# Optimization experiments

Measured on AMD Instinct MI355X. Metric: run time of the kernel, lower is better.

Reference implementation:

```python
import jax, jax.numpy as jnp
import numpy as np

TAU = 2.0          # LIF membrane time constant
VTH = 1.0          # spike threshold
ALPHA = 2.0        # ATan surrogate default alpha
EPS = 1e-5         # LayerNorm eps


@jax.custom_vjp
def atan_spike(x):
    # Heaviside forward, ATan surrogate gradient backward (spikingjelly surrogate.ATan)
    return (x >= 0.0).astype(x.dtype)

def _spike_fwd(x):
    return atan_spike(x), x

def _spike_bwd(x, g):
    sg = (ALPHA / 2.0) / (1.0 + (jnp.pi / 2.0 * ALPHA * x) ** 2)
    return (g * sg,)

atan_spike.defvjp(_spike_fwd, _spike_bwd)


def lif_scan(xs):
    # xs: [T, B, C]; multi-step LIF with decay_input=True, v_reset=0.0 (hard reset),
    # detach_reset=True (reset path is stop_gradient'ed).
    def step(v, x):
        h = v + (x - v) / TAU                      # charge
        s = atan_spike(h - VTH)                    # fire
        v_new = h * (1.0 - jax.lax.stop_gradient(s))  # hard reset to 0, detached
        return v_new, s
    _, spikes = jax.lax.scan(step, jnp.zeros_like(xs[0]), xs)
    return spikes


def setup_inputs() -> dict:
    key = jax.random.key(0)
    ks = jax.random.split(key, 5)
    B, T, D, H = 32, 2048, 128, 256
    x = jax.random.normal(ks[0], (B, T, D), dtype=jnp.float32)
    W1 = jax.random.normal(ks[1], (H, D), dtype=jnp.float32) * (1.0 / np.sqrt(D))
    b1 = jax.random.normal(ks[2], (H,), dtype=jnp.float32) * 0.02
    W2 = jax.random.normal(ks[3], (D, H), dtype=jnp.float32) * (1.0 / np.sqrt(H))
    b2 = jax.random.normal(ks[4], (D,), dtype=jnp.float32) * 0.02
    ln_w = jnp.ones((D,), dtype=jnp.float32)
    ln_b = jnp.zeros((D,), dtype=jnp.float32)
    return {"x": x, "W1": W1, "b1": b1, "W2": W2, "b2": b2, "ln_w": ln_w, "ln_b": ln_b}


def reference(x, W1, b1, W2, b2, ln_w, ln_b):
    # x: [B, T, D] -> time-major [T, B, D]
    h = jnp.swapaxes(x, 0, 1)
    h = h @ W1.T + b1            # [T, B, H]
    h = lif_scan(h)              # spikes in {0,1}
    h = h @ W2.T + b2            # [T, B, D]
    h = lif_scan(h)
    h = jnp.swapaxes(h, 0, 1)    # back to [B, T, D]
    y = x + h                    # residual
    mu = jnp.mean(y, axis=-1, keepdims=True)
    var = jnp.mean((y - mu) ** 2, axis=-1, keepdims=True)
    return (y - mu) * jax.lax.rsqrt(var + EPS) * ln_w + ln_b
```

## Files before the change

### kernel.cpp

```cpp
#include <hip/hip_runtime.h>


typedef _Float16 half8 __attribute__((ext_vector_type(8)));
typedef float f32x4 __attribute__((ext_vector_type(4)));

#define MFMA_F16(a, b, c) __builtin_amdgcn_mfma_f32_16x16x32_f16(a, b, c, 0, 0, 0)

__device__ __forceinline__ unsigned short h2u(_Float16 h) {
    union { _Float16 h; unsigned short u; } x; x.h = h; return x.u;
}

__device__ __forceinline__ void split8(float4 f0, float4 f1, half8& a, half8& b) {
    float fs[8] = {f0.x, f0.y, f0.z, f0.w, f1.x, f1.y, f1.z, f1.w};
    half8 ha, hb;
#pragma unroll
    for (int q = 0; q < 8; ++q) {
        ha[q] = (_Float16)fs[q];
        hb[q] = (_Float16)(fs[q] - (float)ha[q]);
    }
    a = ha; b = hb;
}

__global__ __launch_bounds__(512, 1) void mega_kernel(
    const float* __restrict__ X,
    const float* __restrict__ W1, const float* __restrict__ W2,
    const float* __restrict__ b1, const float* __restrict__ b2,
    const float* __restrict__ lnw, const float* __restrict__ lnb,
    float* __restrict__ out)
{
    __shared__ __align__(16) float h1buf[16 * 260];
    __shared__ __align__(16) float h2buf[16 * 132];
    __shared__ __align__(16) float s2buf[16 * 132];
    __shared__ __align__(16) unsigned short spkbuf[16 * 264];
    __shared__ __align__(16) unsigned short xb[2][16 * 136];

    const int tid = threadIdx.x;
    const int lane = tid & 63;
    const int w = tid >> 6;
    const bool isS = (tid < 256);
    const int sg = w;
    const int gg = w - 4;
    const int fr = lane & 15;
    const int fo8 = (lane >> 4) * 8;
    const int qr = (lane >> 4) * 4;
    const int b = blockIdx.y;
    const int t0 = blockIdx.x * 256;
    const int s0 = (blockIdx.x == 0) ? 8 : 0;

    const float* __restrict__ xbase = X + (size_t)b * 2048 * 128;
    float* __restrict__ obase = out + (size_t)b * 2048 * 128;

    half8 wf[32];
    float bias0[4];
    if (isS) {
#pragma unroll
        for (int j = 0; j < 2; ++j) {
            const size_t d = (size_t)(32 * sg + 16 * j + fr) * 256;
#pragma unroll
            for (int ks = 0; ks < 8; ++ks) {
                float4 f0 = *(const float4*)&W2[d + ks * 32 + fo8];
                float4 f1 = *(const float4*)&W2[d + ks * 32 + fo8 + 4];
                split8(f0, f1, wf[(j * 8 + ks) * 2], wf[(j * 8 + ks) * 2 + 1]);
            }
            bias0[j] = b2[32 * sg + 16 * j + fr];
        }
    } else {
#pragma unroll
        for (int j = 0; j < 4; ++j) {
            const size_t n = (size_t)(64 * gg + 16 * j + fr) * 128;
#pragma unroll
            for (int k0 = 0; k0 < 4; ++k0) {
                float4 f0 = *(const float4*)&W1[n + k0 * 32 + fo8];
                float4 f1 = *(const float4*)&W1[n + k0 * 32 + fo8 + 4];
                split8(f0, f1, wf[(j * 4 + k0) * 2], wf[(j * 4 + k0) * 2 + 1]);
            }
            bias0[j] = b1[64 * gg + 16 * j + fr];
        }
    }
    const float2 wv = *(const float2*)(lnw + lane * 2);
    const float2 bbv = *(const float2*)(lnb + lane * 2);

    float v1 = 0.0f, v2 = 0.0f;
    const int d2 = (tid - 256) & 127;
    const int tgs = (tid - 384) & 127;
    const int srow = tgs >> 5;
    const int sc4 = (tgs & 31) * 4;
    float4 pfx[4];
    float2 pflnC[2], pflnN[2];

    if (tid >= 384) {
        const int tb = t0 - 128 + s0 * 16;
#pragma unroll
        for (int q = 0; q < 4; ++q) {
            float4 xv = *(const float4*)&xbase[(size_t)(tb + srow + 4 * q) * 128 + sc4];
            _Float16 a0 = (_Float16)xv.x, e0 = (_Float16)(xv.x - (float)a0);
            _Float16 a1 = (_Float16)xv.y, e1 = (_Float16)(xv.y - (float)a1);
            _Float16 a2 = (_Float16)xv.z, e2 = (_Float16)(xv.z - (float)a2);
            _Float16 a3 = (_Float16)xv.w, e3 = (_Float16)(xv.w - (float)a3);
            ushort4 ua = {h2u(a0), h2u(a1), h2u(a2), h2u(a3)};
            ushort4 ue = {h2u(e0), h2u(e1), h2u(e2), h2u(e3)};
            *(ushort4*)&xb[0][(srow + 4 * q) * 136 + sc4] = ua;
            *(ushort4*)&xb[1][(srow + 4 * q) * 136 + sc4] = ue;
        }
    }
    __syncthreads();
    if (!isS) {
        const _Float16* xa0 = (const _Float16*)&xb[0][0];
        const _Float16* xa1 = (const _Float16*)&xb[1][0];
        f32x4 acc[4];
#pragma unroll
        for (int j = 0; j < 4; ++j) acc[j] = (f32x4){0.f, 0.f, 0.f, 0.f};
#pragma unroll
        for (int k0 = 0; k0 < 4; ++k0) {
            half8 a0 = *(const half8*)&xa0[fr * 136 + k0 * 32 + fo8];
            half8 a1 = *(const half8*)&xa1[fr * 136 + k0 * 32 + fo8];
#pragma unroll
            for (int j = 0; j < 4; ++j) {
                acc[j] = MFMA_F16(a0, wf[(j * 4 + k0) * 2], acc[j]);
                acc[j] = MFMA_F16(a0, wf[(j * 4 + k0) * 2 + 1], acc[j]);
                acc[j] = MFMA_F16(a1, wf[(j * 4 + k0) * 2], acc[j]);
            }
        }
#pragma unroll
        for (int j = 0; j < 4; ++j) {
            int col = 64 * gg + 16 * j + fr;
#pragma unroll
            for (int r = 0; r < 4; ++r)
                h1buf[(qr + r) * 260 + col] = acc[j][r] + bias0[j];
        }
        if (tid >= 384) {
            const int tb = t0 - 128 + s0 * 16 + 16;
#pragma unroll
            for (int q = 0; q < 4; ++q)
                pfx[q] = *(const float4*)&xbase[(size_t)(tb + srow + 4 * q) * 128 + sc4];
        }
    }
    __syncthreads();

    for (int s = s0; s <= 24; ++s) {
        const int tbase = t0 - 128 + s * 16;

        if (isS) {
            if (s <= 23) {
                float hh[16];
#pragma unroll
                for (int t = 0; t < 16; ++t) hh[t] = h1buf[t * 260 + tid];
#pragma unroll
                for (int t = 0; t < 16; ++t) {
                    float h = v1 + (hh[t] - v1) * 0.5f;
                    bool sp = (h >= 1.0f);
                    v1 = sp ? 0.0f : h;
                    spkbuf[t * 264 + tid] = sp ? (unsigned short)0x3C00 : (unsigned short)0;
                }
            }
        } else if (tid < 384) {
            if (s > s0) {
                float hh[16];
#pragma unroll
                for (int t = 0; t < 16; ++t) hh[t] = h2buf[t * 132 + d2];
#pragma unroll
                for (int t = 0; t < 16; ++t) {
                    float h = v2 + (hh[t] - v2) * 0.5f;
                    bool sp = (h >= 1.0f);
                    v2 = sp ? 0.0f : h;
                    s2buf[t * 132 + d2] = sp ? 1.0f : 0.0f;
                }
            }
        } else {
            if (s <= 22) {
#pragma unroll
                for (int q = 0; q < 4; ++q) {
                    float4 xv = pfx[q];
                    _Float16 a0 = (_Float16)xv.x, e0 = (_Float16)(xv.x - (float)a0);
                    _Float16 a1 = (_Float16)xv.y, e1 = (_Float16)(xv.y - (float)a1);
                    _Float16 a2 = (_Float16)xv.z, e2 = (_Float16)(xv.z - (float)a2);
                    _Float16 a3 = (_Float16)xv.w, e3 = (_Float16)(xv.w - (float)a3);
                    ushort4 ua = {h2u(a0), h2u(a1), h2u(a2), h2u(a3)};
                    ushort4 ue = {h2u(e0), h2u(e1), h2u(e2), h2u(e3)};
                    *(ushort4*)&xb[0][(srow + 4 * q) * 136 + sc4] = ua;
                    *(ushort4*)&xb[1][(srow + 4 * q) * 136 + sc4] = ue;
                }
            }
        }
        __syncthreads();

        if (isS) {
            if (s <= 23) {
                const _Float16* sp = (const _Float16*)&spkbuf[0];
                f32x4 acc[2];
                acc[0] = (f32x4){0.f, 0.f, 0.f, 0.f};
                acc[1] = (f32x4){0.f, 0.f, 0.f, 0.f};
#pragma unroll
                for (int ks = 0; ks < 8; ++ks) {
                    half8 a = *(const half8*)&sp[fr * 264 + ks * 32 + fo8];
#pragma unroll
                    for (int j = 0; j < 2; ++j) {
                        acc[j] = MFMA_F16(a, wf[(j * 8 + ks) * 2], acc[j]);
                        acc[j] = MFMA_F16(a, wf[(j * 8 + ks) * 2 + 1], acc[j]);
                    }
                }
#pragma unroll
                for (int j = 0; j < 2; ++j) {
                    int col = 32 * sg + 16 * j + fr;
#pragma unroll
                    for (int r = 0; r < 4; ++r)
                        h2buf[(qr + r) * 132 + col] = acc[j][r] + bias0[j];
                }
            }
        } else {
            if (s <= 22) {
                const _Float16* xa0 = (const _Float16*)&xb[0][0];
                const _Float16* xa1 = (const _Float16*)&xb[1][0];
                f32x4 acc[4];
#pragma unroll
                for (int j = 0; j < 4; ++j) acc[j] = (f32x4){0.f, 0.f, 0.f, 0.f};
#pragma unroll
                for (int k0 = 0; k0 < 4; ++k0) {
                    half8 a0 = *(const half8*)&xa0[fr * 136 + k0 * 32 + fo8];
                    half8 a1 = *(const half8*)&xa1[fr * 136 + k0 * 32 + fo8];
#pragma unroll
                    for (int j = 0; j < 4; ++j) {
                        acc[j] = MFMA_F16(a0, wf[(j * 4 + k0) * 2], acc[j]);
                        acc[j] = MFMA_F16(a0, wf[(j * 4 + k0) * 2 + 1], acc[j]);
                        acc[j] = MFMA_F16(a1, wf[(j * 4 + k0) * 2], acc[j]);
                    }
                }
#pragma unroll
                for (int j = 0; j < 4; ++j) {
                    int col = 64 * gg + 16 * j + fr;
#pragma unroll
                    for (int r = 0; r < 4; ++r)
                        h1buf[(qr + r) * 260 + col] = acc[j][r] + bias0[j];
                }
            }
            if (tid >= 384 && s <= 21) {
#pragma unroll
                for (int q = 0; q < 4; ++q)
                    pfx[q] = *(const float4*)&xbase[(size_t)(tbase + 32 + srow + 4 * q) * 128 + sc4];
            }
        }

        if (s >= 8 && s <= 23) {
#pragma unroll
            for (int rr = 0; rr < 2; ++rr)
                pflnN[rr] = *(const float2*)&xbase[(size_t)(tbase + 2 * w + rr) * 128 + lane * 2];
        }

        if (s >= 9) {
            const int tbm = tbase - 16;
#pragma unroll
            for (int rr = 0; rr < 2; ++rr) {
                int row = 2 * w + rr;
                float2 s2v = *(const float2*)&s2buf[row * 132 + lane * 2];
                float y0 = pflnC[rr].x + s2v.x;
                float y1 = pflnC[rr].y + s2v.y;
                float sum = y0 + y1;
                float ss = y0 * y0 + y1 * y1;
#pragma unroll
                for (int off = 32; off > 0; off >>= 1) {
                    sum += __shfl_xor(sum, off, 64);
                    ss  += __shfl_xor(ss, off, 64);
                }
                float mu = sum * (1.0f / 128.0f);
                float var = ss * (1.0f / 128.0f) - mu * mu;
                float inv = rsqrtf(var + 1e-5f);
                float2 o;
                o.x = (y0 - mu) * inv * wv.x + bbv.x;
                o.y = (y1 - mu) * inv * wv.y + bbv.y;
                *(float2*)&obase[(size_t)(tbm + row) * 128 + lane * 2] = o;
            }
        }
        pflnC[0] = pflnN[0];
        pflnC[1] = pflnN[1];
        __syncthreads();
    }
}

extern "C" void kernel_launch(void* const* d_in, const int* in_sizes, int n_in,
                              void* d_out, int out_size, void* d_ws, size_t ws_size,
                              hipStream_t stream)
{
    const float* x   = (const float*)d_in[0];
    const float* W1  = (const float*)d_in[1];
    const float* b1  = (const float*)d_in[2];
    const float* W2  = (const float*)d_in[3];
    const float* b2  = (const float*)d_in[4];
    const float* lnw = (const float*)d_in[5];
    const float* lnb = (const float*)d_in[6];
    float* out = (float*)d_out;

    dim3 gM(8, 32);
    mega_kernel<<<gM, 512, 0, stream>>>(x, W1, W2, b1, b2, lnw, lnb, out);
}
```

Baseline: 144.2 us.

## Double-buffer stage buffers to drop one barrier per step and deepen prefetch

```diff
diff --git a/kernel.cpp b/kernel.cpp
--- a/kernel.cpp
+++ b/kernel.cpp
@@ -28,11 +28,11 @@
     const float* __restrict__ lnw, const float* __restrict__ lnb,
     float* __restrict__ out)
 {
-    __shared__ __align__(16) float h1buf[16 * 260];
-    __shared__ __align__(16) float h2buf[16 * 132];
-    __shared__ __align__(16) float s2buf[16 * 132];
-    __shared__ __align__(16) unsigned short spkbuf[16 * 264];
-    __shared__ __align__(16) unsigned short xb[2][16 * 136];
+    __shared__ __align__(16) float h1[2][16 * 260];
+    __shared__ __align__(16) float h2[2][16 * 132];
+    __shared__ __align__(16) float s2[2][16 * 132];
+    __shared__ __align__(16) unsigned short spk[2][16 * 264];
+    __shared__ __align__(16) unsigned short xb[2][2][16 * 136];
 
     const int tid = threadIdx.x;
     const int lane = tid & 63;
@@ -85,28 +85,37 @@
     const int tgs = (tid - 384) & 127;
     const int srow = tgs >> 5;
     const int sc4 = (tgs & 31) * 4;
-    float4 pfx[4];
+    const bool isStage = (tid >= 384);
+    float4 pfxA[4], pfxB[4];
     float2 pflnC[2], pflnN[2];
 
-    if (tid >= 384) {
-        const int tb = t0 - 128 + s0 * 16;
+    auto stage_write = [&](int par, const float4 (&pf)[4]) {
 #pragma unroll
         for (int q = 0; q < 4; ++q) {
-            float4 xv = *(const float4*)&xbase[(size_t)(tb + srow + 4 * q) * 128 + sc4];
+            float4 xv = pf[q];
             _Float16 a0 = (_Float16)xv.x, e0 = (_Float16)(xv.x - (float)a0);
             _Float16 a1 = (_Float16)xv.y, e1 = (_Float16)(xv.y - (float)a1);
             _Float16 a2 = (_Float16)xv.z, e2 = (_Float16)(xv.z - (float)a2);
             _Float16 a3 = (_Float16)xv.w, e3 = (_Float16)(xv.w - (float)a3);
             ushort4 ua = {h2u(a0), h2u(a1), h2u(a2), h2u(a3)};
             ushort4 ue = {h2u(e0), h2u(e1), h2u(e2), h2u(e3)};
-            *(ushort4*)&xb[0][(srow + 4 * q) * 136 + sc4] = ua;
-            *(ushort4*)&xb[1][(srow + 4 * q) * 136 + sc4] = ue;
-        }
+            *(ushort4*)&xb[par][0][(srow + 4 * q) * 136 + sc4] = ua;
+            *(ushort4*)&xb[par][1][(srow + 4 * q) * 136 + sc4] = ue;
+        }
+    };
+
+    if (isStage) {
+        const int tb = t0 - 128 + s0 * 16;
+        float4 pf[4];
+#pragma unroll
+        for (int q = 0; q < 4; ++q)
+            pf[q] = *(const float4*)&xbase[(size_t)(tb + srow + 4 * q) * 128 + sc4];
+        stage_write(s0 & 1, pf);
     }
     __syncthreads();
     if (!isS) {
-        const _Float16* xa0 = (const _Float16*)&xb[0][0];
-        const _Float16* xa1 = (const _Float16*)&xb[1][0];
+        const _Float16* xa0 = (const _Float16*)&xb[s0 & 1][0][0];
+        const _Float16* xa1 = (const _Float16*)&xb[s0 & 1][1][0];
         f32x4 acc[4];
 #pragma unroll
         for (int j = 0; j < 4; ++j) acc[j] = (f32x4){0.f, 0.f, 0.f, 0.f};
@@ -126,67 +135,39 @@
             int col = 64 * gg + 16 * j + fr;
 #pragma unroll
             for (int r = 0; r < 4; ++r)
-                h1buf[(qr + r) * 260 + col] = acc[j][r] + bias0[j];
-        }
-        if (tid >= 384) {
-            const int tb = t0 - 128 + s0 * 16 + 16;
+                h1[s0 & 1][(qr + r) * 260 + col] = acc[j][r] + bias0[j];
+        }
+        if (isStage) {
+            const int tb1 = t0 - 128 + (s0 + 1) * 16;
+            float4 pf[4];
 #pragma unroll
             for (int q = 0; q < 4; ++q)
-                pfx[q] = *(const float4*)&xbase[(size_t)(tb + srow + 4 * q) * 128 + sc4];
+                pf[q] = *(const float4*)&xbase[(size_t)(tb1 + srow + 4 * q) * 128 + sc4];
+            stage_write((s0 + 1) & 1, pf);
+            const int tb2 = t0 - 128 + (s0 + 2) * 16;
+            const int tb3 = t0 - 128 + (s0 + 3) * 16;
+#pragma unroll
+            for (int q = 0; q < 4; ++q) {
+                pfxA[q] = *(const float4*)&xbase[(size_t)(tb2 + srow + 4 * q) * 128 + sc4];
+                pfxB[q] = *(const float4*)&xbase[(size_t)(tb3 + srow + 4 * q) * 128 + sc4];
+            }
         }
     }
     __syncthreads();
 
-    for (int s = s0; s <= 24; ++s) {
-        const int tbase = t0 - 128 + s * 16;
+    for (int ph = s0; ph <= 26; ++ph) {
+        const int tb = t0 - 128 + ph * 16;
+
+        if (ph >= 10 && ph <= 25) {
+#pragma unroll
+            for (int rr = 0; rr < 2; ++rr)
+                pflnN[rr] = *(const float2*)&xbase[(size_t)(tb - 32 + 2 * w + rr) * 128 + lane * 2];
+        }
 
         if (isS) {
-            if (s <= 23) {
-                float hh[16];
-#pragma unroll
-                for (int t = 0; t < 16; ++t) hh[t] = h1buf[t * 260 + tid];
-#pragma unroll
-                for (int t = 0; t < 16; ++t) {
-                    float h = v1 + (hh[t] - v1) * 0.5f;
-                    bool sp = (h >= 1.0f);
-                    v1 = sp ? 0.0f : h;
-                    spkbuf[t * 264 + tid] = sp ? (unsigned short)0x3C00 : (unsigned short)0;
-                }
-            }
-        } else if (tid < 384) {
-            if (s > s0) {
-                float hh[16];
-#pragma unroll
-                for (int t = 0; t < 16; ++t) hh[t] = h2buf[t * 132 + d2];
-#pragma unroll
-                for (int t = 0; t < 16; ++t) {
-                    float h = v2 + (hh[t] - v2) * 0.5f;
-                    bool sp = (h >= 1.0f);
-                    v2 = sp ? 0.0f : h;
-                    s2buf[t * 132 + d2] = sp ? 1.0f : 0.0f;
-                }
-            }
-        } else {
-            if (s <= 22) {
-#pragma unroll
-                for (int q = 0; q < 4; ++q) {
-                    float4 xv = pfx[q];
-                    _Float16 a0 = (_Float16)xv.x, e0 = (_Float16)(xv.x - (float)a0);
-                    _Float16 a1 = (_Float16)xv.y, e1 = (_Float16)(xv.y - (float)a1);
-                    _Float16 a2 = (_Float16)xv.z, e2 = (_Float16)(xv.z - (float)a2);
-                    _Float16 a3 = (_Float16)xv.w, e3 = (_Float16)(xv.w - (float)a3);
-                    ushort4 ua = {h2u(a0), h2u(a1), h2u(a2), h2u(a3)};
-                    ushort4 ue = {h2u(e0), h2u(e1), h2u(e2), h2u(e3)};
-                    *(ushort4*)&xb[0][(srow + 4 * q) * 136 + sc4] = ua;
-                    *(ushort4*)&xb[1][(srow + 4 * q) * 136 + sc4] = ue;
-                }
-            }
-        }
-        __syncthreads();
-
-        if (isS) {
-            if (s <= 23) {
-                const _Float16* sp = (const _Float16*)&spkbuf[0];
+            if (ph >= s0 + 1 && ph <= 24) {
+                const int p = (ph - 1) & 1;
+                const _Float16* sp = (const _Float16*)&spk[p][0];
                 f32x4 acc[2];
                 acc[0] = (f32x4){0.f, 0.f, 0.f, 0.f};
                 acc[1] = (f32x4){0.f, 0.f, 0.f, 0.f};
@@ -204,13 +185,45 @@
                     int col = 32 * sg + 16 * j + fr;
 #pragma unroll
                     for (int r = 0; r < 4; ++r)
-                        h2buf[(qr + r) * 132 + col] = acc[j][r] + bias0[j];
-                }
+                        h2[p][(qr + r) * 132 + col] = acc[j][r] + bias0[j];
+                }
+            }
+            if (ph <= 23) {
+                const int p = ph & 1;
+                float hh[16];
+#pragma unroll
+                for (int t = 0; t < 16; ++t) hh[t] = h1[p][t * 260 + tid];
+                __builtin_amdgcn_s_setprio(1);
+#pragma unroll
+                for (int t = 0; t < 16; ++t) {
+                    float h = v1 + (hh[t] - v1) * 0.5f;
+                    bool sp_ = (h >= 1.0f);
+                    v1 = sp_ ? 0.0f : h;
+                    spk[p][t * 264 + tid] = sp_ ? (unsigned short)0x3C00 : (unsigned short)0;
+                }
+                __builtin_amdgcn_s_setprio(0);
             }
         } else {
-            if (s <= 22) {
-                const _Float16* xa0 = (const _Float16*)&xb[0][0];
-                const _Float16* xa1 = (const _Float16*)&xb[1][0];
+            if (isStage && ph <= 21) {
+                if ((ph & 1) == 0) stage_write(0, pfxA);
+                else               stage_write(1, pfxB);
+            }
+            if (isStage && ph <= 19) {
+                const int tbn = tb + 64;
+                if ((ph & 1) == 0) {
+#pragma unroll
+                    for (int q = 0; q < 4; ++q)
+                        pfxA[q] = *(const float4*)&xbase[(size_t)(tbn + srow + 4 * q) * 128 + sc4];
+                } else {
+#pragma unroll
+                    for (int q = 0; q < 4; ++q)
+                        pfxB[q] = *(const float4*)&xbase[(size_t)(tbn + srow + 4 * q) * 128 + sc4];
+                }
+            }
+            if (ph <= 22) {
+                const int p = (ph + 1) & 1;
+                const _Float16* xa0 = (const _Float16*)&xb[p][0][0];
+                const _Float16* xa1 = (const _Float16*)&xb[p][1][0];
                 f32x4 acc[4];
 #pragma unroll
                 for (int j = 0; j < 4; ++j) acc[j] = (f32x4){0.f, 0.f, 0.f, 0.f};
@@ -230,28 +243,33 @@
                     int col = 64 * gg + 16 * j + fr;
 #pragma unroll
                     for (int r = 0; r < 4; ++r)
-                        h1buf[(qr + r) * 260 + col] = acc[j][r] + bias0[j];
-                }
-            }
-            if (tid >= 384 && s <= 21) {
-#pragma unroll
-                for (int q = 0; q < 4; ++q)
-                    pfx[q] = *(const float4*)&xbase[(size_t)(tbase + 32 + srow + 4 * q) * 128 + sc4];
-            }
-        }
-
-        if (s >= 8 && s <= 23) {
-#pragma unroll
-            for (int rr = 0; rr < 2; ++rr)
-                pflnN[rr] = *(const float2*)&xbase[(size_t)(tbase + 2 * w + rr) * 128 + lane * 2];
-        }
-
-        if (s >= 9) {
-            const int tbm = tbase - 16;
+                        h1[p][(qr + r) * 260 + col] = acc[j][r] + bias0[j];
+                }
+            }
+            if (!isStage && ph >= s0 + 2 && ph <= 25) {
+                const int p = (ph - 2) & 1;
+                float hh[16];
+#pragma unroll
+                for (int t = 0; t < 16; ++t) hh[t] = h2[p][t * 132 + d2];
+                __builtin_amdgcn_s_setprio(1);
+#pragma unroll
+                for (int t = 0; t < 16; ++t) {
+                    float h = v2 + (hh[t] - v2) * 0.5f;
+                    bool sp_ = (h >= 1.0f);
+                    v2 = sp_ ? 0.0f : h;
+                    s2[p][t * 132 + d2] = sp_ ? 1.0f : 0.0f;
+                }
+                __builtin_amdgcn_s_setprio(0);
+            }
+        }
+
+        if (ph >= 11 && ph <= 26) {
+            const int p = (ph - 3) & 1;
+            const int tbm = tb - 48;
 #pragma unroll
             for (int rr = 0; rr < 2; ++rr) {
                 int row = 2 * w + rr;
-                float2 s2v = *(const float2*)&s2buf[row * 132 + lane * 2];
+                float2 s2v = *(const float2*)&s2[p][row * 132 + lane * 2];
                 float y0 = pflnC[rr].x + s2v.x;
                 float y1 = pflnC[rr].y + s2v.y;
                 float sum = y0 + y1;
```

Result: no change. 146.7 us (+1.8%).
